# Optimization experiments

Hardware: AMD Instinct MI355X
Metric: run time of the kernel (lower is better)

## Reference

```python
import jax, jax.numpy as jnp
import numpy as np

N_NODES = 100000
N_EDGES = 1600000
IN_F, HID_F, OUT_F = 64, 64, 64


def setup_inputs() -> dict:
    key = jax.random.key(0)
    ks = jax.random.split(key, 9)
    return {
        "x": jax.random.normal(ks[0], (N_NODES, IN_F), dtype=jnp.float32),
        "src": jax.random.randint(ks[1], (N_EDGES,), 0, N_NODES, dtype=jnp.int64),
        "dst": jax.random.randint(ks[2], (N_EDGES,), 0, N_NODES, dtype=jnp.int64),
        "W_self1": jax.random.normal(ks[3], (IN_F, HID_F), dtype=jnp.float32) * (1.0 / np.sqrt(IN_F)),
        "W_neigh1": jax.random.normal(ks[4], (IN_F, HID_F), dtype=jnp.float32) * (1.0 / np.sqrt(IN_F)),
        "b1": jnp.zeros((HID_F,), dtype=jnp.float32),
        "W_self2": jax.random.normal(ks[5], (HID_F, OUT_F), dtype=jnp.float32) * (1.0 / np.sqrt(HID_F)),
        "W_neigh2": jax.random.normal(ks[6], (HID_F, OUT_F), dtype=jnp.float32) * (1.0 / np.sqrt(HID_F)),
        "b2": jnp.zeros((OUT_F,), dtype=jnp.float32),
    }


def reference(x, src, dst, W_self1, W_neigh1, b1, W_self2, W_neigh2, b2):
    N = x.shape[0]
    # in-degree per destination node; zero-in-degree nodes get zero aggregate (DGL semantics)
    deg = jax.ops.segment_sum(jnp.ones(dst.shape, dtype=x.dtype), dst, num_segments=N)
    inv_deg = jnp.where(deg > 0, 1.0 / jnp.maximum(deg, 1.0), 0.0)[:, None]  # [N,1]

    def sage_conv(h, W_s, W_n, b):
        # mean over in-neighbors: gather src feats, segment-sum at dst, normalize
        agg = jax.ops.segment_sum(h[src], dst, num_segments=N) * inv_deg  # [N,F]
        return h @ W_s + agg @ W_n + b

    h = jax.nn.relu(sage_conv(x, W_self1, W_neigh1, b1))
    return sage_conv(h, W_self2, W_neigh2, b2)
```

## Files before the change

### kernel.cpp

```cpp
#include <hip/hip_runtime.h>

#define N_NODES 100000
#define N_EDGES 1600000
#define NBKT 196
#define BKT_SHIFT 9
#define BKT_MASK 511

typedef __attribute__((ext_vector_type(8))) short short8;
typedef __attribute__((ext_vector_type(4))) float float4v;

__device__ __forceinline__ unsigned short f2bf(float f) {
  unsigned u = __float_as_uint(f);
  return (unsigned short)((u + 0x7fffu + ((u >> 16) & 1u)) >> 16);
}
__device__ __forceinline__ float bflo(unsigned d) { return __uint_as_float(d << 16); }
__device__ __forceinline__ float bfhi(unsigned d) { return __uint_as_float(d & 0xffff0000u); }


__global__ void kA_count(const int* __restrict__ dst, int* __restrict__ blkCnt) {
  __shared__ int hist[NBKT];
  for (int t = threadIdx.x; t < NBKT; t += 256) hist[t] = 0;
  __syncthreads();
  const int chunk = (N_EDGES + gridDim.x - 1) / gridDim.x;
  const int e0 = blockIdx.x * chunk;
  const int e1 = min(e0 + chunk, N_EDGES);
  for (int e = e0 + threadIdx.x; e < e1; e += 256)
    atomicAdd(&hist[dst[e] >> BKT_SHIFT], 1);
  __syncthreads();
  for (int t = threadIdx.x; t < NBKT; t += 256)
    blkCnt[t * 256 + blockIdx.x] = hist[t];
}

__global__ void kA_scan1(int* __restrict__ blkCnt, int* __restrict__ bktTot) {
  const int b = blockIdx.x;
  const int tid = threadIdx.x, lane = tid & 63, w = tid >> 6;
  int v = blkCnt[b * 256 + tid];
  int inc = v;
  #pragma unroll
  for (int d = 1; d < 64; d <<= 1) { int y = __shfl_up(inc, d); if (lane >= d) inc += y; }
  __shared__ int wtot[4];
  if (lane == 63) wtot[w] = inc;
  __syncthreads();
  int base = 0;
  for (int j = 0; j < w; j++) base += wtot[j];
  blkCnt[b * 256 + tid] = base + inc - v;
  if (tid == 255) bktTot[b] = base + inc;
}

__global__ void kA_scan2(const int* __restrict__ bktTot, int* __restrict__ bktStart) {
  int lane = threadIdx.x;
  int running = 0;
  for (int base = 0; base < NBKT; base += 64) {
    int i = base + lane;
    int v = (i < NBKT) ? bktTot[i] : 0;
    int inc = v;
    #pragma unroll
    for (int d = 1; d < 64; d <<= 1) { int y = __shfl_up(inc, d); if (lane >= d) inc += y; }
    if (i < NBKT) bktStart[i] = running + inc - v;
    running += __shfl(inc, 63);
  }
}

__global__ void kA_scatter(const int* __restrict__ src, const int* __restrict__ dst,
                           const int* __restrict__ blkCnt, const int* __restrict__ bktStart,
                           int* __restrict__ binned) {
  __shared__ int curb[NBKT];
  for (int t = threadIdx.x; t < NBKT; t += 256)
    curb[t] = bktStart[t] + blkCnt[t * 256 + blockIdx.x];
  __syncthreads();
  const int chunk = (N_EDGES + gridDim.x - 1) / gridDim.x;
  const int e0 = blockIdx.x * chunk;
  const int e1 = min(e0 + chunk, N_EDGES);
  for (int e = e0 + threadIdx.x; e < e1; e += 256) {
    int d = dst[e];
    int s = src[e];
    int b = d >> BKT_SHIFT;
    int p = atomicAdd(&curb[b], 1);
    binned[p] = s | ((d & BKT_MASK) << 17);
  }
}


__global__ void k_sort(const int* __restrict__ binned, const int* __restrict__ bktStart,
                       const int* __restrict__ bktTot,
                       int* __restrict__ off, int* __restrict__ esrc) {
  const int b = blockIdx.x;
  const int tid = threadIdx.x, lane = tid & 63, w = tid >> 6;
  __shared__ int cnt[512];
  __shared__ int pos[512];
  cnt[tid] = 0; cnt[tid + 256] = 0;
  __syncthreads();
  const int s0 = bktStart[b], ne = bktTot[b];
  for (int i = tid; i < ne; i += 256)
    atomicAdd(&cnt[binned[s0 + i] >> 17], 1);
  __syncthreads();
  int c0 = cnt[2 * tid], c1 = cnt[2 * tid + 1];
  int v = c0 + c1;
  int inc = v;
  #pragma unroll
  for (int d = 1; d < 64; d <<= 1) { int y = __shfl_up(inc, d); if (lane >= d) inc += y; }
  __shared__ int wtot[4];
  if (lane == 63) wtot[w] = inc;
  __syncthreads();
  int base = s0;
  for (int j = 0; j < w; j++) base += wtot[j];
  int ex = base + inc - v;
  pos[2 * tid] = ex;
  pos[2 * tid + 1] = ex + c0;
  int n0 = (b << BKT_SHIFT) + 2 * tid;
  if (n0 < N_NODES)     off[n0] = ex;
  if (n0 + 1 < N_NODES) off[n0 + 1] = ex + c0;
  if (b == NBKT - 1 && tid == 0) off[N_NODES] = N_EDGES;
  __syncthreads();
  for (int i = tid; i < ne; i += 256) {
    int pe = binned[s0 + i];
    int p = atomicAdd(&pos[pe >> 17], 1);
    esrc[p] = pe & 0x1FFFF;
  }
}


__global__ void k_cvt(const float* __restrict__ in, unsigned short* __restrict__ outb) {
  int i = blockIdx.x * blockDim.x + threadIdx.x;
  const int n4 = (N_NODES * 64) / 4;
  if (i < n4) {
    float4 v = ((const float4*)in)[i];
    unsigned d0 = ((unsigned)f2bf(v.y) << 16) | f2bf(v.x);
    unsigned d1 = ((unsigned)f2bf(v.w) << 16) | f2bf(v.z);
    ((uint2*)outb)[i] = make_uint2(d0, d1);
  }
}


__global__ void k_wprep(const float* __restrict__ W0, const float* __restrict__ W1,
                        const float* __restrict__ W2, const float* __restrict__ W3,
                        unsigned short* __restrict__ F) {
  const float* W = (blockIdx.x == 0) ? W0 : (blockIdx.x == 1) ? W1
                 : (blockIdx.x == 2) ? W2 : W3;
  unsigned short* out = F + blockIdx.x * 4096;
  int lane = threadIdx.x;
  int col = lane & 15, kr = lane >> 4;
  #pragma unroll
  for (int kc = 0; kc < 2; kc++)
    #pragma unroll
    for (int nt = 0; nt < 4; nt++) {
      unsigned d[4];
      #pragma unroll
      for (int jj = 0; jj < 4; jj++) {
        float w0 = W[(kc * 32 + kr * 8 + 2 * jj)     * 64 + nt * 16 + col];
        float w1 = W[(kc * 32 + kr * 8 + 2 * jj + 1) * 64 + nt * 16 + col];
        d[jj] = ((unsigned)f2bf(w1) << 16) | f2bf(w0);
      }
      uint4* p = (uint4*)(out + ((kc * 4 + nt) * 64 + lane) * 8);
      *p = make_uint4(d[0], d[1], d[2], d[3]);
    }
}


__global__ void k_agg(const unsigned short* __restrict__ featb,
                      const int* __restrict__ off, const int* __restrict__ esrc,
                      unsigned short* __restrict__ aggb) {
  const int lane = threadIdx.x & 63;
  const int r = lane >> 3;
  const int c = lane & 7;
  const int wid = (blockIdx.x * blockDim.x + threadIdx.x) >> 6;
  const int nw  = (gridDim.x * blockDim.x) >> 6;

  for (int n = wid; n < N_NODES; n += nw) {
    const int o0 = off[n], o1 = off[n + 1];
    float acc[8];
    #pragma unroll
    for (int j = 0; j < 8; j++) acc[j] = 0.f;

    int i = o0;
    for (; i + 16 <= o1; i += 16) {
      int sA = esrc[i + r];
      int sB = esrc[i + 8 + r];
      uint4 vA = *(const uint4*)(featb + sA * 64 + c * 8);
      uint4 vB = *(const uint4*)(featb + sB * 64 + c * 8);
      acc[0] += bflo(vA.x); acc[1] += bfhi(vA.x);
      acc[2] += bflo(vA.y); acc[3] += bfhi(vA.y);
      acc[4] += bflo(vA.z); acc[5] += bfhi(vA.z);
      acc[6] += bflo(vA.w); acc[7] += bfhi(vA.w);
      acc[0] += bflo(vB.x); acc[1] += bfhi(vB.x);
      acc[2] += bflo(vB.y); acc[3] += bfhi(vB.y);
      acc[4] += bflo(vB.z); acc[5] += bfhi(vB.z);
      acc[6] += bflo(vB.w); acc[7] += bfhi(vB.w);
    }
    if (i + 8 <= o1) {
      int s = esrc[i + r];
      uint4 v = *(const uint4*)(featb + s * 64 + c * 8);
      acc[0] += bflo(v.x); acc[1] += bfhi(v.x);
      acc[2] += bflo(v.y); acc[3] += bfhi(v.y);
      acc[4] += bflo(v.z); acc[5] += bfhi(v.z);
      acc[6] += bflo(v.w); acc[7] += bfhi(v.w);
      i += 8;
    }
    if (i < o1) {
      int e = i + r;
      if (e < o1) {
        int s = esrc[e];
        uint4 v = *(const uint4*)(featb + s * 64 + c * 8);
        acc[0] += bflo(v.x); acc[1] += bfhi(v.x);
        acc[2] += bflo(v.y); acc[3] += bfhi(v.y);
        acc[4] += bflo(v.z); acc[5] += bfhi(v.z);
        acc[6] += bflo(v.w); acc[7] += bfhi(v.w);
      }
    }
    #pragma unroll
    for (int m = 8; m <= 32; m <<= 1)
      #pragma unroll
      for (int j = 0; j < 8; j++) acc[j] += __shfl_xor(acc[j], m);

    const int dg = o1 - o0;
    const float inv = (dg > 0) ? (1.0f / (float)dg) : 0.f;
    if (r == 0) {
      unsigned d0 = ((unsigned)f2bf(acc[1] * inv) << 16) | f2bf(acc[0] * inv);
      unsigned d1 = ((unsigned)f2bf(acc[3] * inv) << 16) | f2bf(acc[2] * inv);
      unsigned d2 = ((unsigned)f2bf(acc[5] * inv) << 16) | f2bf(acc[4] * inv);
      unsigned d3 = ((unsigned)f2bf(acc[7] * inv) << 16) | f2bf(acc[6] * inv);
      *(uint4*)(aggb + n * 64 + c * 8) = make_uint4(d0, d1, d2, d3);
    }
  }
}


template <bool RELU, bool OUT_BF>
__global__ void k_xform(const unsigned short* __restrict__ selfb,
                        const unsigned short* __restrict__ aggb,
                        const unsigned short* __restrict__ wfS,
                        const unsigned short* __restrict__ wfN,
                        const float* __restrict__ bias,
                        float* __restrict__ outf, unsigned short* __restrict__ outb) {
  const int lane = threadIdx.x & 63;
  const int col = lane & 15, rr = lane >> 4;
  const int wid = (blockIdx.x * blockDim.x + threadIdx.x) >> 6;
  const int nw  = (gridDim.x * blockDim.x) >> 6;

  short8 bs[2][4], bn[2][4];
  #pragma unroll
  for (int kc = 0; kc < 2; kc++)
    #pragma unroll
    for (int nt = 0; nt < 4; nt++) {
      bs[kc][nt] = *(const short8*)(wfS + ((kc * 4 + nt) * 64 + lane) * 8);
      bn[kc][nt] = *(const short8*)(wfN + ((kc * 4 + nt) * 64 + lane) * 8);
    }
  float bv[4];
  #pragma unroll
  for (int nt = 0; nt < 4; nt++) bv[nt] = bias[nt * 16 + col];

  const int NT = N_NODES / 16;
  for (int t = wid; t < NT; t += nw) {
    const int m = t * 16 + col;
    short8 as0 = *(const short8*)(selfb + m * 64 + rr * 8);
    short8 as1 = *(const short8*)(selfb + m * 64 + 32 + rr * 8);
    short8 aa0 = *(const short8*)(aggb + m * 64 + rr * 8);
    short8 aa1 = *(const short8*)(aggb + m * 64 + 32 + rr * 8);
    #pragma unroll
    for (int nt = 0; nt < 4; nt++) {
      float4v cfr = {bv[nt], bv[nt], bv[nt], bv[nt]};
      cfr = __builtin_amdgcn_mfma_f32_16x16x32_bf16(as0, bs[0][nt], cfr, 0, 0, 0);
      cfr = __builtin_amdgcn_mfma_f32_16x16x32_bf16(as1, bs[1][nt], cfr, 0, 0, 0);
      cfr = __builtin_amdgcn_mfma_f32_16x16x32_bf16(aa0, bn[0][nt], cfr, 0, 0, 0);
      cfr = __builtin_amdgcn_mfma_f32_16x16x32_bf16(aa1, bn[1][nt], cfr, 0, 0, 0);
      #pragma unroll
      for (int r2 = 0; r2 < 4; r2++) {
        int row = t * 16 + rr * 4 + r2;
        float v = cfr[r2];
        if (RELU) v = fmaxf(v, 0.f);
        if (OUT_BF) outb[row * 64 + nt * 16 + col] = f2bf(v);
        else        outf[row * 64 + nt * 16 + col] = v;
      }
    }
  }
}


extern "C" void kernel_launch(void* const* d_in, const int* in_sizes, int n_in,
                              void* d_out, int out_size, void* d_ws, size_t ws_size,
                              hipStream_t stream) {
  const float* x   = (const float*)d_in[0];
  const int*   src = (const int*)d_in[1];
  const int*   dst = (const int*)d_in[2];
  const float* Ws1 = (const float*)d_in[3];
  const float* Wn1 = (const float*)d_in[4];
  const float* b1  = (const float*)d_in[5];
  const float* Ws2 = (const float*)d_in[6];
  const float* Wn2 = (const float*)d_in[7];
  const float* b2  = (const float*)d_in[8];

  char* ws = (char*)d_ws;
  int*            blkCnt   = (int*)(ws + 0);
  int*            bktTot   = (int*)(ws + 262144);
  int*            bktStart = (int*)(ws + 266240);
  unsigned short* wf       = (unsigned short*)(ws + 270336);
  int*            binned   = (int*)(ws + 303104);
  int*            off      = (int*)(ws + 6703104);
  int*            esrc     = (int*)(ws + 7103488);
  unsigned short* xbf      = (unsigned short*)(ws + 13503488);
  unsigned short* hbf      = (unsigned short*)(ws + 26303488);
  unsigned short* agg1     = (unsigned short*)(ws + 39103488);
  unsigned short* agg2     = (unsigned short*)(ws + 51903488);

  kA_count<<<256, 256, 0, stream>>>(dst, blkCnt);
  kA_scan1<<<NBKT, 256, 0, stream>>>(blkCnt, bktTot);
  kA_scan2<<<1, 64, 0, stream>>>(bktTot, bktStart);
  kA_scatter<<<256, 256, 0, stream>>>(src, dst, blkCnt, bktStart, binned);
  k_sort<<<NBKT, 256, 0, stream>>>(binned, bktStart, bktTot, off, esrc);

  k_cvt<<<(N_NODES * 16 + 255) / 256, 256, 0, stream>>>(x, xbf);
  k_wprep<<<4, 64, 0, stream>>>(Ws1, Wn1, Ws2, Wn2, wf);

  k_agg<<<2048, 256, 0, stream>>>(xbf, off, esrc, agg1);
  k_xform<true, true><<<1024, 256, 0, stream>>>(xbf, agg1, wf + 0 * 4096, wf + 1 * 4096,
                                                b1, nullptr, hbf);
  k_agg<<<2048, 256, 0, stream>>>(hbf, off, esrc, agg2);
  k_xform<false, false><<<1024, 256, 0, stream>>>(hbf, agg2, wf + 2 * 4096, wf + 3 * 4096,
                                                  b2, (float*)d_out, nullptr);
}
```

Before: 242.9 us.

## Fuse neighbor aggregation with MFMA transform via per-wave LDS tiles

Merges the aggregation and transform kernels so each wave aggregates 16 destination nodes into a swizzled LDS tile, then immediately runs the bf16 MFMA transform on that tile. This removes the global round-trip of the aggregate buffers and two kernel launches. It also merges the feature conversion and weight prep into one launch. In exchange, each wave handles exactly one tile with no grid-stride loop and reloads the weight fragments per tile, and degree imbalance within a tile can leave waves unevenly loaded.

```diff
diff --git a/kernel.cpp b/kernel.cpp
--- a/kernel.cpp
+++ b/kernel.cpp
@@ -5,6 +5,7 @@
 #define NBKT 196
 #define BKT_SHIFT 9
 #define BKT_MASK 511
+#define NT_TILES 6250
 
 typedef __attribute__((ext_vector_type(8))) short short8;
 typedef __attribute__((ext_vector_type(4))) float float4v;
@@ -120,24 +121,22 @@
 }
 
 
-__global__ void k_cvt(const float* __restrict__ in, unsigned short* __restrict__ outb) {
-  int i = blockIdx.x * blockDim.x + threadIdx.x;
-  const int n4 = (N_NODES * 64) / 4;
-  if (i < n4) {
+__global__ void k_prep(const float* __restrict__ in, unsigned short* __restrict__ outb,
+                       const float* __restrict__ W0, const float* __restrict__ W1,
+                       const float* __restrict__ W2, const float* __restrict__ W3,
+                       unsigned short* __restrict__ F) {
+  if (blockIdx.x < NT_TILES) {
+    int i = blockIdx.x * 256 + threadIdx.x;
     float4 v = ((const float4*)in)[i];
     unsigned d0 = ((unsigned)f2bf(v.y) << 16) | f2bf(v.x);
     unsigned d1 = ((unsigned)f2bf(v.w) << 16) | f2bf(v.z);
     ((uint2*)outb)[i] = make_uint2(d0, d1);
-  }
-}
-
-
-__global__ void k_wprep(const float* __restrict__ W0, const float* __restrict__ W1,
-                        const float* __restrict__ W2, const float* __restrict__ W3,
-                        unsigned short* __restrict__ F) {
-  const float* W = (blockIdx.x == 0) ? W0 : (blockIdx.x == 1) ? W1
-                 : (blockIdx.x == 2) ? W2 : W3;
-  unsigned short* out = F + blockIdx.x * 4096;
+    return;
+  }
+  if (threadIdx.x >= 64) return;
+  const int wsel = blockIdx.x - NT_TILES;
+  const float* W = (wsel == 0) ? W0 : (wsel == 1) ? W1 : (wsel == 2) ? W2 : W3;
+  unsigned short* out = F + wsel * 4096;
   int lane = threadIdx.x;
   int col = lane & 15, kr = lane >> 4;
   #pragma unroll
@@ -157,20 +156,31 @@
 }
 
 
-__global__ void k_agg(const unsigned short* __restrict__ featb,
-                      const int* __restrict__ off, const int* __restrict__ esrc,
-                      unsigned short* __restrict__ aggb) {
-  const int lane = threadIdx.x & 63;
+template <bool RELU, bool OUT_BF>
+__global__ void k_fused(const unsigned short* __restrict__ featb,
+                        const int* __restrict__ off, const int* __restrict__ esrc,
+                        const unsigned short* __restrict__ wfS,
+                        const unsigned short* __restrict__ wfN,
+                        const float* __restrict__ bias,
+                        float* __restrict__ outf, unsigned short* __restrict__ outb) {
+  __shared__ unsigned short aggl[4][16 * 64];
+  const int tid = threadIdx.x;
+  const int lane = tid & 63;
+  const int wslot = tid >> 6;
+  const int t = (blockIdx.x * blockDim.x + tid) >> 6;
+  if (t >= NT_TILES) return;
+
+  unsigned short* lw = &aggl[wslot][0];
   const int r = lane >> 3;
   const int c = lane & 7;
-  const int wid = (blockIdx.x * blockDim.x + threadIdx.x) >> 6;
-  const int nw  = (gridDim.x * blockDim.x) >> 6;
-
-  for (int n = wid; n < N_NODES; n += nw) {
-    const int o0 = off[n], o1 = off[n + 1];
+
+  int o1 = off[t * 16];
+  for (int j = 0; j < 16; ++j) {
+    const int o0 = o1;
+    o1 = off[t * 16 + j + 1];
     float acc[8];
     #pragma unroll
-    for (int j = 0; j < 8; j++) acc[j] = 0.f;
+    for (int q = 0; q < 8; q++) acc[q] = 0.f;
 
     int i = o0;
     for (; i + 16 <= o1; i += 16) {
@@ -210,7 +220,7 @@
     #pragma unroll
     for (int m = 8; m <= 32; m <<= 1)
       #pragma unroll
-      for (int j = 0; j < 8; j++) acc[j] += __shfl_xor(acc[j], m);
+      for (int q = 0; q < 8; q++) acc[q] += __shfl_xor(acc[q], m);
 
     const int dg = o1 - o0;
     const float inv = (dg > 0) ? (1.0f / (float)dg) : 0.f;
@@ -219,58 +229,39 @@
       unsigned d1 = ((unsigned)f2bf(acc[3] * inv) << 16) | f2bf(acc[2] * inv);
       unsigned d2 = ((unsigned)f2bf(acc[5] * inv) << 16) | f2bf(acc[4] * inv);
       unsigned d3 = ((unsigned)f2bf(acc[7] * inv) << 16) | f2bf(acc[6] * inv);
-      *(uint4*)(aggb + n * 64 + c * 8) = make_uint4(d0, d1, d2, d3);
-    }
-  }
-}
-
-
-template <bool RELU, bool OUT_BF>
-__global__ void k_xform(const unsigned short* __restrict__ selfb,
-                        const unsigned short* __restrict__ aggb,
-                        const unsigned short* __restrict__ wfS,
-                        const unsigned short* __restrict__ wfN,
-                        const float* __restrict__ bias,
-                        float* __restrict__ outf, unsigned short* __restrict__ outb) {
-  const int lane = threadIdx.x & 63;
+      *(uint4*)(lw + j * 64 + ((c ^ (j & 7)) << 3)) = make_uint4(d0, d1, d2, d3);
+    }
+  }
+
+  __builtin_amdgcn_wave_barrier();
+  asm volatile("" ::: "memory");
+
   const int col = lane & 15, rr = lane >> 4;
-  const int wid = (blockIdx.x * blockDim.x + threadIdx.x) >> 6;
-  const int nw  = (gridDim.x * blockDim.x) >> 6;
-
-  short8 bs[2][4], bn[2][4];
+  const int m = t * 16 + col;
+  short8 as0 = *(const short8*)(featb + m * 64 + rr * 8);
+  short8 as1 = *(const short8*)(featb + m * 64 + 32 + rr * 8);
+  short8 aa0 = *(const short8*)(lw + col * 64 + ((rr ^ (col & 7)) << 3));
+  short8 aa1 = *(const short8*)(lw + col * 64 + (((rr + 4) ^ (col & 7)) << 3));
+
   #pragma unroll
-  for (int kc = 0; kc < 2; kc++)
-    #pragma unroll
-    for (int nt = 0; nt < 4; nt++) {
-      bs[kc][nt] = *(const short8*)(wfS + ((kc * 4 + nt) * 64 + lane) * 8);
-      bn[kc][nt] = *(const short8*)(wfN + ((kc * 4 + nt) * 64 + lane) * 8);
-    }
-  float bv[4];
-  #pragma unroll
-  for (int nt = 0; nt < 4; nt++) bv[nt] = bias[nt * 16 + col];
-
-  const int NT = N_NODES / 16;
-  for (int t = wid; t < NT; t += nw) {
-    const int m = t * 16 + col;
-    short8 as0 = *(const short8*)(selfb + m * 64 + rr * 8);
-    short8 as1 = *(const short8*)(selfb + m * 64 + 32 + rr * 8);
-    short8 aa0 = *(const short8*)(aggb + m * 64 + rr * 8);
-    short8 aa1 = *(const short8*)(aggb + m * 64 + 32 + rr * 8);
-    #pragma unroll
-    for (int nt = 0; nt < 4; nt++) {
-      float4v cfr = {bv[nt], bv[nt], bv[nt], bv[nt]};
-      cfr = __builtin_amdgcn_mfma_f32_16x16x32_bf16(as0, bs[0][nt], cfr, 0, 0, 0);
-      cfr = __builtin_amdgcn_mfma_f32_16x16x32_bf16(as1, bs[1][nt], cfr, 0, 0, 0);
-      cfr = __builtin_amdgcn_mfma_f32_16x16x32_bf16(aa0, bn[0][nt], cfr, 0, 0, 0);
-      cfr = __builtin_amdgcn_mfma_f32_16x16x32_bf16(aa1, bn[1][nt], cfr, 0, 0, 0);
-      #pragma unroll
-      for (int r2 = 0; r2 < 4; r2++) {
-        int row = t * 16 + rr * 4 + r2;
-        float v = cfr[r2];
-        if (RELU) v = fmaxf(v, 0.f);
-        if (OUT_BF) outb[row * 64 + nt * 16 + col] = f2bf(v);
-        else        outf[row * 64 + nt * 16 + col] = v;
-      }
+  for (int nt = 0; nt < 4; nt++) {
+    short8 bs0 = *(const short8*)(wfS + ((0 * 4 + nt) * 64 + lane) * 8);
+    short8 bs1 = *(const short8*)(wfS + ((1 * 4 + nt) * 64 + lane) * 8);
+    short8 bn0 = *(const short8*)(wfN + ((0 * 4 + nt) * 64 + lane) * 8);
+    short8 bn1 = *(const short8*)(wfN + ((1 * 4 + nt) * 64 + lane) * 8);
+    float bvn = bias[nt * 16 + col];
+    float4v cfr = {bvn, bvn, bvn, bvn};
+    cfr = __builtin_amdgcn_mfma_f32_16x16x32_bf16(as0, bs0, cfr, 0, 0, 0);
+    cfr = __builtin_amdgcn_mfma_f32_16x16x32_bf16(as1, bs1, cfr, 0, 0, 0);
+    cfr = __builtin_amdgcn_mfma_f32_16x16x32_bf16(aa0, bn0, cfr, 0, 0, 0);
+    cfr = __builtin_amdgcn_mfma_f32_16x16x32_bf16(aa1, bn1, cfr, 0, 0, 0);
+    #pragma unroll
+    for (int r2 = 0; r2 < 4; r2++) {
+      int row = t * 16 + rr * 4 + r2;
+      float v = cfr[r2];
+      if (RELU) v = fmaxf(v, 0.f);
+      if (OUT_BF) outb[row * 64 + nt * 16 + col] = f2bf(v);
+      else        outf[row * 64 + nt * 16 + col] = v;
     }
   }
 }
@@ -299,8 +290,6 @@
   int*            esrc     = (int*)(ws + 7103488);
   unsigned short* xbf      = (unsigned short*)(ws + 13503488);
   unsigned short* hbf      = (unsigned short*)(ws + 26303488);
-  unsigned short* agg1     = (unsigned short*)(ws + 39103488);
-  unsigned short* agg2     = (unsigned short*)(ws + 51903488);
 
   kA_count<<<256, 256, 0, stream>>>(dst, blkCnt);
   kA_scan1<<<NBKT, 256, 0, stream>>>(blkCnt, bktTot);
@@ -308,13 +297,10 @@
   kA_scatter<<<256, 256, 0, stream>>>(src, dst, blkCnt, bktStart, binned);
   k_sort<<<NBKT, 256, 0, stream>>>(binned, bktStart, bktTot, off, esrc);
 
-  k_cvt<<<(N_NODES * 16 + 255) / 256, 256, 0, stream>>>(x, xbf);
-  k_wprep<<<4, 64, 0, stream>>>(Ws1, Wn1, Ws2, Wn2, wf);
-
-  k_agg<<<2048, 256, 0, stream>>>(xbf, off, esrc, agg1);
-  k_xform<true, true><<<1024, 256, 0, stream>>>(xbf, agg1, wf + 0 * 4096, wf + 1 * 4096,
-                                                b1, nullptr, hbf);
-  k_agg<<<2048, 256, 0, stream>>>(hbf, off, esrc, agg2);
-  k_xform<false, false><<<1024, 256, 0, stream>>>(hbf, agg2, wf + 2 * 4096, wf + 3 * 4096,
-                                                  b2, (float*)d_out, nullptr);
-}
+  k_prep<<<NT_TILES + 4, 256, 0, stream>>>(x, xbf, Ws1, Wn1, Ws2, Wn2, wf);
+
+  k_fused<true, true><<<1563, 256, 0, stream>>>(xbf, off, esrc, wf + 0 * 4096,
+                                                wf + 1 * 4096, b1, nullptr, hbf);
+  k_fused<false, false><<<1563, 256, 0, stream>>>(hbf, off, esrc, wf + 2 * 4096,
+                                                  wf + 3 * 4096, b2, (float*)d_out, nullptr);
+}
```

Measured after the change: 238.6 us. About the same (-1.8%).
